# Performance work log

Measured on AMD Instinct MI355X. Metric: run time of the kernel, lower is better.

Reference implementation:

```python
import jax, jax.numpy as jnp
import numpy as np

B, T, I, R, O = 64, 2048, 25, 512, 50
ALPHA = 0.5
RHO = 0.99


def setup_inputs() -> dict:
    key = jax.random.key(0)
    k1, k2, k3, k4 = jax.random.split(key, 4)
    x = jax.random.normal(k1, (B, T, I), dtype=jnp.float32)
    Win = jax.random.uniform(k2, (R, I), minval=-0.1, maxval=0.1, dtype=jnp.float32)
    W = jax.random.normal(k3, (R, R), dtype=jnp.float32) * 0.1
    sr_actual = np.max(np.abs(np.linalg.eigvals(np.asarray(W))))
    W = W / jnp.float32(sr_actual) * jnp.float32(RHO)
    Wout = jax.random.normal(k4, (O, R), dtype=jnp.float32) * 0.1
    return {"x": x, "Win": Win, "W": W, "Wout": Wout}


def reference(x, Win, W, Wout):
    a = jnp.asarray(ALPHA, dtype=x.dtype)
    # Precompute input projections for all timesteps (batched GEMM).
    xin = jnp.einsum('bti,ri->btr', x, Win)  # [B, T, R]

    def step(h, u):
        # h: [B, R], u: [B, R]
        h = (1 - a) * h + a * jnp.tanh(u + h @ W.T)
        return h, h

    h0 = jnp.zeros((x.shape[0], W.shape[0]), dtype=x.dtype)
    _, states = jax.lax.scan(step, h0, jnp.swapaxes(xin, 0, 1))  # [T, B, R]
    states = jnp.swapaxes(states, 0, 1)  # [B, T, R]
    return states @ Wout.T  # [B, T, O]
```

## Files before the change

kernel.cpp:

```cpp
#include <hip/hip_runtime.h>
#include <math.h>


typedef float v2f __attribute__((ext_vector_type(2)));
typedef float v4f __attribute__((ext_vector_type(4)));

template<int CTRL>
__device__ __forceinline__ float dpp_add(float x) {
    int y = __builtin_amdgcn_update_dpp(0, __float_as_int(x), CTRL, 0xF, 0xF, false);
    return x + __int_as_float(y);
}

__device__ __forceinline__ void store_ic8(float* p, float h, int tag) {
    v2f v; v[0] = h; v[1] = __int_as_float(tag);
    asm volatile("global_store_dwordx2 %0, %1, off sc0 sc1"
                 :: "v"(p), "v"(v) : "memory");
}
__device__ __forceinline__ void load3_ic(const float* p0, const float* p1,
                                         const float* p2, v4f& a, v4f& b, v4f& c) {
    asm volatile("global_load_dwordx4 %0, %3, off sc0 sc1\n\t"
                 "global_load_dwordx4 %1, %4, off sc0 sc1\n\t"
                 "global_load_dwordx4 %2, %5, off sc0 sc1\n\t"
                 "s_waitcnt vmcnt(0)"
                 : "=&v"(a), "=&v"(b), "=&v"(c)
                 : "v"(p0), "v"(p1), "v"(p2) : "memory");
}
__device__ __forceinline__ void load3_l2(const float* p0, const float* p1,
                                         const float* p2, v4f& a, v4f& b, v4f& c) {
    asm volatile("global_load_dwordx4 %0, %3, off sc0\n\t"
                 "global_load_dwordx4 %1, %4, off sc0\n\t"
                 "global_load_dwordx4 %2, %5, off sc0\n\t"
                 "s_waitcnt vmcnt(0)"
                 : "=&v"(a), "=&v"(b), "=&v"(c)
                 : "v"(p0), "v"(p1), "v"(p2) : "memory");
}

__device__ __forceinline__ int permidx(int c) {
    return (c >> 7) * 128 + (c & 31) * 4 + ((c >> 5) & 3);
}

#define TAGS_BAD (__any((__float_as_int(d0.y) != want) | (__float_as_int(d0.w) != want) | \
                        (__float_as_int(d1.y) != want) | (__float_as_int(d1.w) != want) | \
                        (__float_as_int(d2.y) != want) | (__float_as_int(d2.w) != want)))

__global__ void __launch_bounds__(512, 2)
esn_kernel(const float* __restrict__ x, const float* __restrict__ Win,
           const float* __restrict__ W, const float* __restrict__ Wout,
           float* __restrict__ out, float* __restrict__ Hf)
{
    const int b    = blockIdx.x & 63;
    const int g    = blockIdx.x >> 6;
    const int tid  = threadIdx.x;
    const int rt   = tid >> 5;
    const int ct   = tid & 31;
    const int lane = tid & 63;
    const int wv   = tid >> 6;
    const int hw   = rt & 1;

    __shared__ __align__(16) float hperm[2][512];

    v2f Wreg[64];
    {
        const int i0 = g*128 + rt*8;
        #pragma unroll
        for (int r = 0; r < 4; ++r)
        #pragma unroll
        for (int q = 0; q < 4; ++q) {
            const float* wp = W + (r*128 + q*32 + ct);
            #pragma unroll
            for (int p = 0; p < 4; ++p) {
                v2f w;
                w[0] = wp[(size_t)(i0 + 2*p    ) * 512];
                w[1] = wp[(size_t)(i0 + 2*p + 1) * 512];
                Wreg[(r*4+q)*4 + p] = w;
            }
        }
    }

    const int myrow = g*128 + rt*8 + (ct & 7);
    float WinR[25];
    #pragma unroll
    for (int k = 0; k < 25; ++k) WinR[k] = Win[myrow*25 + k];

    const int obase = g*13;
    const int ocnt  = (g == 3) ? 11 : 13;
    const int oloc  = 2*wv + hw;
    const bool ovalid = (oloc < ocnt);
    const int oidx  = obase + (ovalid ? oloc : 0);
    float WoutR[16];
    #pragma unroll
    for (int r = 0; r < 4; ++r)
    #pragma unroll
    for (int q = 0; q < 4; ++q)
        WoutR[r*4+q] = ovalid ? Wout[oidx*512 + r*128 + q*32 + ct] : 0.f;

    hperm[0][tid] = 0.f;
    float holdv = 0.f;
    const bool fin = (ct >= 16) & (ct < 24);

    const float* xrow = x   + (size_t)b * 2048 * 25;
    float*       orow = out + (size_t)b * 2048 * 50;
    float* HfB0 = Hf + (size_t)b * 1024;
    const int s0 = (g+1)&3, s1 = (g+2)&3, s2 = (g+3)&3;

    bool fast = true;

    __syncthreads();

    float u = 0.f;
    #pragma unroll
    for (int k = 0; k < 25; ++k) u = fmaf(WinR[k], xrow[k], u);

    for (int t = 0; t < 2048; ++t) {
        const int par  = t & 1;
        const int npar = par ^ 1;
        const int want = t + 1;
        float* HfN = HfB0 + (size_t)npar * 64 * 1024;

        v2f acc0 = {0.f,0.f}, acc1 = {0.f,0.f}, acc2 = {0.f,0.f}, acc3 = {0.f,0.f};
        float op = 0.f;
        #pragma unroll
        for (int r = 0; r < 4; ++r) {
            v4f hv = *(const v4f*)&hperm[par][r*128 + ct*4];
            #pragma unroll
            for (int q = 0; q < 4; ++q) {
                const float hs = hv[q];
                op = fmaf(WoutR[r*4+q], hs, op);
                v2f hh = {hs, hs};
                acc0 = __builtin_elementwise_fma(Wreg[(r*4+q)*4+0], hh, acc0);
                acc1 = __builtin_elementwise_fma(Wreg[(r*4+q)*4+1], hh, acc1);
                acc2 = __builtin_elementwise_fma(Wreg[(r*4+q)*4+2], hh, acc2);
                acc3 = __builtin_elementwise_fma(Wreg[(r*4+q)*4+3], hh, acc3);
            }
        }

        float ar[8] = {acc0[0],acc0[1],acc1[0],acc1[1],acc2[0],acc2[1],acc3[0],acc3[1]};
        #pragma unroll
        for (int j = 0; j < 8; ++j) {
            ar[j] = dpp_add<0xB1>(ar[j]);
            ar[j] = dpp_add<0x4E>(ar[j]);
            ar[j] = dpp_add<0x124>(ar[j]);
            ar[j] = dpp_add<0x128>(ar[j]);
            ar[j] = dpp_add<0x142>(ar[j]);
        }

        if (fin) {
            const int j = ct & 7;
            float y = ar[0];
            if (j == 1) y = ar[1];
            if (j == 2) y = ar[2];
            if (j == 3) y = ar[3];
            if (j == 4) y = ar[4];
            if (j == 5) y = ar[5];
            if (j == 6) y = ar[6];
            if (j == 7) y = ar[7];
            const float z  = u + y;
            const float e  = __expf(2.f * z);
            const float th = 1.f - 2.f * __builtin_amdgcn_rcpf(e + 1.f);
            holdv = 0.5f * holdv + 0.5f * th;
            hperm[npar][permidx(myrow)] = holdv;
            store_ic8(&HfN[myrow*2], holdv, want);
        }

        op = dpp_add<0xB1>(op);  op = dpp_add<0x4E>(op);
        op = dpp_add<0x124>(op); op = dpp_add<0x128>(op);
        op = dpp_add<0x142>(op);
        if (t > 0 && ovalid && ((lane & 31) == 31))
            orow[(size_t)(t-1)*50 + oidx] = op;
        {
            const int tt = (t < 2047) ? t + 1 : 2047;
            float un = 0.f;
            #pragma unroll
            for (int k = 0; k < 25; ++k) un = fmaf(WinR[k], xrow[tt*25 + k], un);
            u = un;
        }

        if (wv == 0) {
            const float* p0 = HfN + (s0*256 + lane*4);
            const float* p1 = HfN + (s1*256 + lane*4);
            const float* p2 = HfN + (s2*256 + lane*4);
            v4f d0, d1, d2;
            if (fast) {
                const int budget = (t == 0) ? 2048 : 64;
                int tries = 0;
                do { load3_l2(p0, p1, p2, d0, d1, d2); } while (TAGS_BAD && ++tries < budget);
                if (TAGS_BAD) fast = false;
            }
            if (!fast) {
                do { load3_ic(p0, p1, p2, d0, d1, d2); } while (TAGS_BAD);
            }
            const int c0 = s0*128 + 2*lane, c1 = s1*128 + 2*lane, c2 = s2*128 + 2*lane;
            hperm[npar][permidx(c0)]     = d0.x;
            hperm[npar][permidx(c0 + 1)] = d0.z;
            hperm[npar][permidx(c1)]     = d1.x;
            hperm[npar][permidx(c1 + 1)] = d1.z;
            hperm[npar][permidx(c2)]     = d2.x;
            hperm[npar][permidx(c2 + 1)] = d2.z;
        }
        __syncthreads();
    }

    {
        float op = 0.f;
        #pragma unroll
        for (int r = 0; r < 4; ++r) {
            v4f hv = *(const v4f*)&hperm[0][r*128 + ct*4];
            #pragma unroll
            for (int q = 0; q < 4; ++q) op = fmaf(WoutR[r*4+q], hv[q], op);
        }
        op = dpp_add<0xB1>(op);  op = dpp_add<0x4E>(op);
        op = dpp_add<0x124>(op); op = dpp_add<0x128>(op);
        op = dpp_add<0x142>(op);
        if (ovalid && ((lane & 31) == 31))
            orow[(size_t)2047*50 + oidx] = op;
    }
}

extern "C" void kernel_launch(void* const* d_in, const int* in_sizes, int n_in,
                              void* d_out, int out_size, void* d_ws, size_t ws_size,
                              hipStream_t stream)
{
    (void)in_sizes; (void)n_in; (void)out_size; (void)ws_size;
    const float* x    = (const float*)d_in[0];
    const float* Win  = (const float*)d_in[1];
    const float* W    = (const float*)d_in[2];
    const float* Wout = (const float*)d_in[3];
    float* out = (float*)d_out;
    float* Hf  = (float*)d_ws;
    esn_kernel<<<dim3(256), dim3(512), 0, stream>>>(x, Win, W, Wout, out, Hf);
}
```

Before: 3.087 ms.

## Stage block hidden state in LDS and publish via single wave wide store

Each block's 128 new state values now go into a small LDS staging buffer. After a barrier, wave 7 publishes them to the global exchange buffer with one 16-byte tagged store per lane, instead of 128 scattered 8-byte stores from many waves. Output-projection duty moves off wave 0, the poller, so that wave spends less time on non-critical work. The x loads for the next step are issued early and the output reduction is deferred until after the exchange. This adds a second barrier per timestep and a custom lgkm-wait barrier in exchange for better-coalesced cross-block publication and better overlap.

```diff
diff --git a/kernel.cpp b/kernel.cpp
--- a/kernel.cpp
+++ b/kernel.cpp
@@ -11,9 +11,10 @@
     return x + __int_as_float(y);
 }
 
-__device__ __forceinline__ void store_ic8(float* p, float h, int tag) {
-    v2f v; v[0] = h; v[1] = __int_as_float(tag);
-    asm volatile("global_store_dwordx2 %0, %1, off sc0 sc1"
+__device__ __forceinline__ void store_ic16(float* p, float h0, float h1, int tag) {
+    v4f v; v[0] = h0; v[1] = __int_as_float(tag);
+    v[2] = h1; v[3] = __int_as_float(tag);
+    asm volatile("global_store_dwordx4 %0, %1, off sc0 sc1"
                  :: "v"(p), "v"(v) : "memory");
 }
 __device__ __forceinline__ void load3_ic(const float* p0, const float* p1,
@@ -42,6 +43,10 @@
 #define TAGS_BAD (__any((__float_as_int(d0.y) != want) | (__float_as_int(d0.w) != want) | \
                         (__float_as_int(d1.y) != want) | (__float_as_int(d1.w) != want) | \
                         (__float_as_int(d2.y) != want) | (__float_as_int(d2.w) != want)))
+
+#define BAR_LGKM() do { \
+    asm volatile("s_waitcnt lgkmcnt(0)" ::: "memory"); \
+    __builtin_amdgcn_s_barrier(); } while (0)
 
 __global__ void __launch_bounds__(512, 2)
 esn_kernel(const float* __restrict__ x, const float* __restrict__ Win,
@@ -58,6 +63,7 @@
     const int hw   = rt & 1;
 
     __shared__ __align__(16) float hperm[2][512];
+    __shared__ __align__(8)  float hstage[128];
 
     v2f Wreg[64];
     {
@@ -84,8 +90,8 @@
 
     const int obase = g*13;
     const int ocnt  = (g == 3) ? 11 : 13;
-    const int oloc  = 2*wv + hw;
-    const bool ovalid = (oloc < ocnt);
+    const int oloc  = 2*wv - 2 + hw;
+    const bool ovalid = (wv != 0) & (oloc < ocnt);
     const int oidx  = obase + (ovalid ? oloc : 0);
     float WoutR[16];
     #pragma unroll
@@ -116,6 +122,15 @@
         const int npar = par ^ 1;
         const int want = t + 1;
         float* HfN = HfB0 + (size_t)npar * 64 * 1024;
+
+        if (wv == 7) asm volatile("s_waitcnt vmcnt(2)" ::: "memory");
+
+        float xv[25];
+        {
+            const int tt = (t < 2047) ? t + 1 : 2047;
+            #pragma unroll
+            for (int k = 0; k < 25; ++k) xv[k] = xrow[tt*25 + k];
+        }
 
         v2f acc0 = {0.f,0.f}, acc1 = {0.f,0.f}, acc2 = {0.f,0.f}, acc3 = {0.f,0.f};
         float op = 0.f;
@@ -143,6 +158,10 @@
             ar[j] = dpp_add<0x128>(ar[j]);
             ar[j] = dpp_add<0x142>(ar[j]);
         }
+
+        float un = 0.f;
+        #pragma unroll
+        for (int k = 0; k < 25; ++k) un = fmaf(WinR[k], xv[k], un);
 
         if (fin) {
             const int j = ct & 7;
@@ -159,20 +178,16 @@
             const float th = 1.f - 2.f * __builtin_amdgcn_rcpf(e + 1.f);
             holdv = 0.5f * holdv + 0.5f * th;
             hperm[npar][permidx(myrow)] = holdv;
-            store_ic8(&HfN[myrow*2], holdv, want);
-        }
-
-        op = dpp_add<0xB1>(op);  op = dpp_add<0x4E>(op);
-        op = dpp_add<0x124>(op); op = dpp_add<0x128>(op);
-        op = dpp_add<0x142>(op);
-        if (t > 0 && ovalid && ((lane & 31) == 31))
-            orow[(size_t)(t-1)*50 + oidx] = op;
-        {
-            const int tt = (t < 2047) ? t + 1 : 2047;
-            float un = 0.f;
-            #pragma unroll
-            for (int k = 0; k < 25; ++k) un = fmaf(WinR[k], xrow[tt*25 + k], un);
-            u = un;
+            hstage[rt*8 + (ct & 7)]     = holdv;
+        }
+        u = un;
+
+        BAR_LGKM();
+
+        if (wv == 7) {
+            const float h0 = hstage[2*lane];
+            const float h1 = hstage[2*lane + 1];
+            store_ic16(&HfN[(size_t)(g*128 + 2*lane)*2], h0, h1, want);
         }
 
         if (wv == 0) {
@@ -197,7 +212,14 @@
             hperm[npar][permidx(c2)]     = d2.x;
             hperm[npar][permidx(c2 + 1)] = d2.z;
         }
-        __syncthreads();
+
+        op = dpp_add<0xB1>(op);  op = dpp_add<0x4E>(op);
+        op = dpp_add<0x124>(op); op = dpp_add<0x128>(op);
+        op = dpp_add<0x142>(op);
+        if (t > 0 && ovalid && ((lane & 31) == 31))
+            orow[(size_t)(t-1)*50 + oidx] = op;
+
+        BAR_LGKM();
     }
 
     {
```

Result: slower. 4.226 ms (+36.9%).

## Restructure recurrence step to overlap global exchange with compute and lighten barrier

Applied to the files above, without the earlier changes.

The recurrence step is reordered. Wave 0 no longer computes output projections and instead issues its neighbor-state loads before its own tagged store. The input-projection loads for the next step are issued early so their latency hides behind the matvec. __syncthreads is replaced by an LDS-only wait plus s_barrier, with manual vmcnt waits placed so outstanding output stores do not block the barrier. The aim is to shorten the serial critical path of each timestep, at the cost of fragile hand-tuned waitcnt ordering assumptions.

```diff
diff --git a/kernel.cpp b/kernel.cpp
--- a/kernel.cpp
+++ b/kernel.cpp
@@ -34,6 +34,19 @@
                  : "=&v"(a), "=&v"(b), "=&v"(c)
                  : "v"(p0), "v"(p1), "v"(p2) : "memory");
 }
+__device__ __forceinline__ void load3_l2_issue(const float* p0, const float* p1,
+                                               const float* p2, v4f& a, v4f& b, v4f& c) {
+    asm volatile("global_load_dwordx4 %0, %3, off sc0\n\t"
+                 "global_load_dwordx4 %1, %4, off sc0\n\t"
+                 "global_load_dwordx4 %2, %5, off sc0"
+                 : "=&v"(a), "=&v"(b), "=&v"(c)
+                 : "v"(p0), "v"(p1), "v"(p2) : "memory");
+}
+__device__ __forceinline__ void wait_vm1(v4f& a, v4f& b, v4f& c) {
+    asm volatile("s_waitcnt vmcnt(1)"
+                 : "+v"(a), "+v"(b), "+v"(c) :: "memory");
+    __builtin_amdgcn_sched_barrier(0);
+}
 
 __device__ __forceinline__ int permidx(int c) {
     return (c >> 7) * 128 + (c & 31) * 4 + ((c >> 5) & 3);
@@ -42,6 +55,10 @@
 #define TAGS_BAD (__any((__float_as_int(d0.y) != want) | (__float_as_int(d0.w) != want) | \
                         (__float_as_int(d1.y) != want) | (__float_as_int(d1.w) != want) | \
                         (__float_as_int(d2.y) != want) | (__float_as_int(d2.w) != want)))
+
+#define BAR_LGKM() do { \
+    asm volatile("s_waitcnt lgkmcnt(0)" ::: "memory"); \
+    __builtin_amdgcn_s_barrier(); } while (0)
 
 __global__ void __launch_bounds__(512, 2)
 esn_kernel(const float* __restrict__ x, const float* __restrict__ Win,
@@ -77,15 +94,16 @@
         }
     }
 
-    const int myrow = g*128 + rt*8 + (ct & 7);
+    const int myrow  = g*128 + rt*8 + (ct & 7);
+    const int pmyrow = permidx(myrow);
     float WinR[25];
     #pragma unroll
     for (int k = 0; k < 25; ++k) WinR[k] = Win[myrow*25 + k];
 
     const int obase = g*13;
     const int ocnt  = (g == 3) ? 11 : 13;
-    const int oloc  = 2*wv + hw;
-    const bool ovalid = (oloc < ocnt);
+    const int oloc  = 2*wv - 2 + hw;
+    const bool ovalid = (wv != 0) & (oloc >= 0) & (oloc < ocnt);
     const int oidx  = obase + (ovalid ? oloc : 0);
     float WoutR[16];
     #pragma unroll
@@ -116,6 +134,18 @@
         const int npar = par ^ 1;
         const int want = t + 1;
         float* HfN = HfB0 + (size_t)npar * 64 * 1024;
+
+        if (wv != 0) {
+            if (g == 3 && wv == 7) asm volatile("s_waitcnt vmcnt(1)" ::: "memory");
+            else                   asm volatile("s_waitcnt vmcnt(2)" ::: "memory");
+        }
+
+        float xv[25];
+        {
+            const int tt = (t < 2047) ? t + 1 : 2047;
+            #pragma unroll
+            for (int k = 0; k < 25; ++k) xv[k] = xrow[tt*25 + k];
+        }
 
         v2f acc0 = {0.f,0.f}, acc1 = {0.f,0.f}, acc2 = {0.f,0.f}, acc3 = {0.f,0.f};
         float op = 0.f;
@@ -143,6 +173,10 @@
             ar[j] = dpp_add<0x128>(ar[j]);
             ar[j] = dpp_add<0x142>(ar[j]);
         }
+
+        float un = 0.f;
+        #pragma unroll
+        for (int k = 0; k < 25; ++k) un = fmaf(WinR[k], xv[k], un);
 
         if (fin) {
             const int j = ct & 7;
@@ -158,32 +192,23 @@
             const float e  = __expf(2.f * z);
             const float th = 1.f - 2.f * __builtin_amdgcn_rcpf(e + 1.f);
             holdv = 0.5f * holdv + 0.5f * th;
-            hperm[npar][permidx(myrow)] = holdv;
-            store_ic8(&HfN[myrow*2], holdv, want);
-        }
-
-        op = dpp_add<0xB1>(op);  op = dpp_add<0x4E>(op);
-        op = dpp_add<0x124>(op); op = dpp_add<0x128>(op);
-        op = dpp_add<0x142>(op);
-        if (t > 0 && ovalid && ((lane & 31) == 31))
-            orow[(size_t)(t-1)*50 + oidx] = op;
-        {
-            const int tt = (t < 2047) ? t + 1 : 2047;
-            float un = 0.f;
-            #pragma unroll
-            for (int k = 0; k < 25; ++k) un = fmaf(WinR[k], xrow[tt*25 + k], un);
-            u = un;
-        }
+            hperm[npar][pmyrow] = holdv;
+        }
+        u = un;
 
         if (wv == 0) {
             const float* p0 = HfN + (s0*256 + lane*4);
             const float* p1 = HfN + (s1*256 + lane*4);
             const float* p2 = HfN + (s2*256 + lane*4);
             v4f d0, d1, d2;
+            load3_l2_issue(p0, p1, p2, d0, d1, d2);
+            if (fin) store_ic8(&HfN[myrow*2], holdv, want);
+            wait_vm1(d0, d1, d2);
             if (fast) {
                 const int budget = (t == 0) ? 2048 : 64;
                 int tries = 0;
-                do { load3_l2(p0, p1, p2, d0, d1, d2); } while (TAGS_BAD && ++tries < budget);
+                while (TAGS_BAD && ++tries < budget)
+                    load3_l2(p0, p1, p2, d0, d1, d2);
                 if (TAGS_BAD) fast = false;
             }
             if (!fast) {
@@ -196,8 +221,16 @@
             hperm[npar][permidx(c1 + 1)] = d1.z;
             hperm[npar][permidx(c2)]     = d2.x;
             hperm[npar][permidx(c2 + 1)] = d2.z;
-        }
-        __syncthreads();
+        } else {
+            if (fin) store_ic8(&HfN[myrow*2], holdv, want);
+            op = dpp_add<0xB1>(op);  op = dpp_add<0x4E>(op);
+            op = dpp_add<0x124>(op); op = dpp_add<0x128>(op);
+            op = dpp_add<0x142>(op);
+            if (t > 0 && ovalid && ((lane & 31) == 31))
+                orow[(size_t)(t-1)*50 + oidx] = op;
+        }
+
+        BAR_LGKM();
     }
 
     {
```

Measured after the change: 4.209 ms. 36.4% more time.
